# Optimization experiments

Measured on AMD Instinct MI355X. Metric: run time of the kernel, lower is better.

## Reference

```python
import jax, jax.numpy as jnp
import numpy as np

NUM_NODES = 100000
EMBED_DIM = 256
NUM_EDGES = 16384
TOTAL = 524288  # total flattened hyperedge membership entries


def setup_inputs() -> dict:
    key = jax.random.key(0)
    k1, k2, k3 = jax.random.split(key, 3)
    node_embeddings = jax.random.normal(k1, (NUM_NODES, EMBED_DIM), dtype=jnp.float32)
    node_indices = jax.random.randint(k2, (TOTAL,), 0, NUM_NODES, dtype=jnp.int64)
    segment_ids = jnp.sort(jax.random.randint(k3, (TOTAL,), 0, NUM_EDGES, dtype=jnp.int64))
    return {"node_embeddings": node_embeddings, "node_indices": node_indices, "segment_ids": segment_ids}


def reference(node_embeddings, node_indices, segment_ids):
    # Gather member-node embeddings: [TOTAL, D]
    gathered = node_embeddings[node_indices]
    # Segmented sum over hyperedges: [NUM_EDGES, D]
    seg_sum = jax.ops.segment_sum(gathered, segment_ids, num_segments=NUM_EDGES)
    # Per-hyperedge member counts for the mean; guard empty segments.
    counts = jax.ops.segment_sum(jnp.ones((gathered.shape[0],), dtype=gathered.dtype),
                                 segment_ids, num_segments=NUM_EDGES)
    counts = jnp.maximum(counts, 1.0)
    return seg_sum / counts[:, None]
```

## Files before the change

### kernel.cpp

```cpp
#include <hip/hip_runtime.h>


#define EMBED_DIM 256
#define NUM_EDGES 16384
#define TOTAL_MEM 524288

__global__ __launch_bounds__(256) void hyperedge_agg_kernel(
    const float* __restrict__ emb,
    const int*   __restrict__ node_idx,
    const int*   __restrict__ seg_ids,
    float*       __restrict__ out)
{
    const int wave = threadIdx.x >> 6;
    const int lane = threadIdx.x & 63;
    const int seg  = blockIdx.x * 4 + wave;
    if (seg >= NUM_EDGES) return;

    int lo = 0, hi = TOTAL_MEM;
    while (lo < hi) {
        int mid = (lo + hi) >> 1;
        if (seg_ids[mid] < seg) lo = mid + 1; else hi = mid;
    }
    const int start = lo;
    hi = TOTAL_MEM;
    while (lo < hi) {
        int mid = (lo + hi) >> 1;
        if (seg_ids[mid] < seg + 1) lo = mid + 1; else hi = mid;
    }
    const int end = lo;

    float4 acc = make_float4(0.f, 0.f, 0.f, 0.f);
    for (int i = start; i < end; ++i) {
        const int n = node_idx[i];
        const float4* row = (const float4*)(emb + (long long)n * EMBED_DIM);
        float4 v = row[lane];
        acc.x += v.x; acc.y += v.y; acc.z += v.z; acc.w += v.w;
    }

    const float cnt = (end > start) ? (float)(end - start) : 1.0f;
    acc.x /= cnt; acc.y /= cnt; acc.z /= cnt; acc.w /= cnt;

    ((float4*)(out + (long long)seg * EMBED_DIM))[lane] = acc;
}

extern "C" void kernel_launch(void* const* d_in, const int* in_sizes, int n_in,
                              void* d_out, int out_size, void* d_ws, size_t ws_size,
                              hipStream_t stream) {
    const float* emb      = (const float*)d_in[0];
    const int*   node_idx = (const int*)d_in[1];
    const int*   seg_ids  = (const int*)d_in[2];
    float*       out      = (float*)d_out;

    const int blocks = NUM_EDGES / 4;
    hyperedge_agg_kernel<<<blocks, 256, 0, stream>>>(emb, node_idx, seg_ids, out);
}
```

Before: 234.6 us.

## Precompute segment offsets and batch-prefetch gathered rows per wave

Adds a pre-pass kernel that writes segment start offsets into the workspace, so the aggregation kernel no longer runs two binary searches per segment. The aggregation kernel loads up to 64 node indices per wave at once, broadcasts them with shuffles, and issues up to 8 independent row loads before accumulating, which raises memory-level parallelism. It adds an extra kernel launch and depends on the workspace being large enough; otherwise it falls back to the old binary-search kernel.

```diff
diff --git a/kernel.cpp b/kernel.cpp
--- a/kernel.cpp
+++ b/kernel.cpp
@@ -5,7 +5,68 @@
 #define NUM_EDGES 16384
 #define TOTAL_MEM 524288
 
+__global__ __launch_bounds__(256) void seg_bounds_kernel(
+    const int* __restrict__ seg_ids,
+    int*       __restrict__ seg_start)
+{
+    const int i = blockIdx.x * blockDim.x + threadIdx.x;
+    if (i >= TOTAL_MEM) return;
+    const int cur  = seg_ids[i];
+    const int prev = (i == 0) ? -1 : seg_ids[i - 1];
+    for (int s = prev + 1; s <= cur; ++s) seg_start[s] = i;
+    if (i == TOTAL_MEM - 1) {
+        for (int s = cur + 1; s <= NUM_EDGES; ++s) seg_start[s] = TOTAL_MEM;
+    }
+}
+
 __global__ __launch_bounds__(256) void hyperedge_agg_kernel(
+    const float* __restrict__ emb,
+    const int*   __restrict__ node_idx,
+    const int*   __restrict__ seg_start,
+    float*       __restrict__ out)
+{
+    const int wave = threadIdx.x >> 6;
+    const int lane = threadIdx.x & 63;
+    const int seg  = blockIdx.x * 4 + wave;
+    if (seg >= NUM_EDGES) return;
+
+    const int start = seg_start[seg];
+    const int end   = seg_start[seg + 1];
+
+    float4 acc = make_float4(0.f, 0.f, 0.f, 0.f);
+
+    int i = start;
+    while (i < end) {
+        const int batch = min(end - i, 64);
+        const int my = (lane < batch) ? node_idx[i + lane] : 0;
+
+        for (int j = 0; j < batch; j += 8) {
+            const int m = min(batch - j, 8);
+            int ns[8];
+            #pragma unroll
+            for (int t = 0; t < 8; ++t) ns[t] = __shfl(my, j + t);
+            float4 v[8];
+            #pragma unroll
+            for (int t = 0; t < 8; ++t)
+                if (t < m)
+                    v[t] = ((const float4*)(emb + (size_t)ns[t] * EMBED_DIM))[lane];
+            #pragma unroll
+            for (int t = 0; t < 8; ++t)
+                if (t < m) {
+                    acc.x += v[t].x; acc.y += v[t].y;
+                    acc.z += v[t].z; acc.w += v[t].w;
+                }
+        }
+        i += batch;
+    }
+
+    const float cnt = (end > start) ? (float)(end - start) : 1.0f;
+    acc.x /= cnt; acc.y /= cnt; acc.z /= cnt; acc.w /= cnt;
+
+    ((float4*)(out + (size_t)seg * EMBED_DIM))[lane] = acc;
+}
+
+__global__ __launch_bounds__(256) void hyperedge_agg_bsearch_kernel(
     const float* __restrict__ emb,
     const int*   __restrict__ node_idx,
     const int*   __restrict__ seg_ids,
@@ -32,15 +93,12 @@
     float4 acc = make_float4(0.f, 0.f, 0.f, 0.f);
     for (int i = start; i < end; ++i) {
         const int n = node_idx[i];
-        const float4* row = (const float4*)(emb + (long long)n * EMBED_DIM);
-        float4 v = row[lane];
+        float4 v = ((const float4*)(emb + (size_t)n * EMBED_DIM))[lane];
         acc.x += v.x; acc.y += v.y; acc.z += v.z; acc.w += v.w;
     }
-
     const float cnt = (end > start) ? (float)(end - start) : 1.0f;
     acc.x /= cnt; acc.y /= cnt; acc.z /= cnt; acc.w /= cnt;
-
-    ((float4*)(out + (long long)seg * EMBED_DIM))[lane] = acc;
+    ((float4*)(out + (size_t)seg * EMBED_DIM))[lane] = acc;
 }
 
 extern "C" void kernel_launch(void* const* d_in, const int* in_sizes, int n_in,
@@ -51,6 +109,12 @@
     const int*   seg_ids  = (const int*)d_in[2];
     float*       out      = (float*)d_out;
 
-    const int blocks = NUM_EDGES / 4;
-    hyperedge_agg_kernel<<<blocks, 256, 0, stream>>>(emb, node_idx, seg_ids, out);
+    const size_t bounds_bytes = (size_t)(NUM_EDGES + 1) * sizeof(int);
+    if (ws_size >= bounds_bytes) {
+        int* seg_start = (int*)d_ws;
+        seg_bounds_kernel<<<(TOTAL_MEM + 255) / 256, 256, 0, stream>>>(seg_ids, seg_start);
+        hyperedge_agg_kernel<<<NUM_EDGES / 4, 256, 0, stream>>>(emb, node_idx, seg_start, out);
+    } else {
+        hyperedge_agg_bsearch_kernel<<<NUM_EDGES / 4, 256, 0, stream>>>(emb, node_idx, seg_ids, out);
+    }
 }
```

New measurement: 205.2 us. 12.5% less time.
